# Optimization experiments

Measured on AMD Instinct MI355X. Metric: run time of the kernel, lower is better.

Reference implementation:

```python
import jax, jax.numpy as jnp
import numpy as np
import math

N = 768; C_S = 384; C_Z = 128; H = 12; C = 16; P_QK = 4; P_V = 8; C_Z4 = C_Z // 4
INF = 1e5; EPS = 1e-8; LN_EPS = 1e-5


def setup_inputs() -> dict:
    key = jax.random.key(0)
    ks = jax.random.split(key, 16)
    w = lambda k, shp, sc=0.02: jax.random.normal(k, shp, jnp.float32) * sc
    s = jax.random.normal(ks[0], (N, C_S), jnp.float32)
    z = jax.random.normal(ks[1], (N, N, C_Z), jnp.float32)
    m = jax.random.normal(ks[2], (N, 3, 3), jnp.float32)
    q, r_ = jnp.linalg.qr(m)
    rot = q * jnp.sign(jnp.diagonal(r_, axis1=-2, axis2=-1))[:, None, :]  # orthonormal frames
    trans = jax.random.normal(ks[3], (N, 3), jnp.float32) * 10.0
    return {
        "s": s, "z": z, "rot": rot, "trans": trans,
        "s_mask": jnp.ones((N,), jnp.float32),
        "g_s": jnp.ones((C_S,), jnp.float32), "b_s": jnp.zeros((C_S,), jnp.float32),
        "g_z": jnp.ones((C_Z,), jnp.float32), "b_z": jnp.zeros((C_Z,), jnp.float32),
        "Wq": w(ks[4], (C_S, H * C)), "Wk": w(ks[5], (C_S, H * C)), "Wv": w(ks[6], (C_S, H * C)),
        "Wqp": w(ks[7], (C_S, H * P_QK * 3)), "Wkp": w(ks[8], (C_S, H * P_QK * 3)),
        "Wvp": w(ks[9], (C_S, H * P_V * 3)),
        "Wb": w(ks[10], (C_Z, H)), "Wdz": w(ks[11], (C_Z, C_Z4)),
        "head_weights": jnp.zeros((H,), jnp.float32),
        "Wout": w(ks[12], (H * C, C_S)), "Woutb": w(ks[13], (H * C_Z4, C_S)),
        "Woutpts": w(ks[14], (H * P_V * 4, C_S)),
        "rigids_to_res_idx": jnp.arange(N, dtype=jnp.int32),
    }


def _ipa(s, z, rot, trans, s_mask, g_s, b_s, g_z, b_z, Wq, Wk, Wv, Wqp, Wkp, Wvp,
         Wb, Wdz, head_weights, Wout, Woutb, Woutpts, idx):
    def ln(x, g, b):
        mu = jnp.mean(x, -1, keepdims=True)
        var = jnp.mean((x - mu) ** 2, -1, keepdims=True)
        return (x - mu) * jax.lax.rsqrt(var + LN_EPS) * g + b

    s = ln(s, g_s, b_s)
    z = ln(z, g_z, b_z)
    n = s.shape[0]
    q = (s @ Wq).reshape(n, H, C)
    k = (s @ Wk).reshape(n, H, C)
    v = (s @ Wv).reshape(n, H, C)

    def to_global(pts):  # r.apply: R x + t, per residue
        return jnp.einsum('nij,npj->npi', rot, pts) + trans[:, None, :]

    q_pts = to_global((s @ Wqp).reshape(n, H * P_QK, 3))
    k_pts = to_global((s @ Wkp).reshape(n, H * P_QK, 3))
    v_pts = to_global((s @ Wvp).reshape(n, H * P_V, 3))

    b = z @ Wb                      # [N, N, H] pair bias
    pair_z = z @ Wdz                # [N, N, C_Z4]
    mask2 = s_mask[:, None] * s_mask[None, :]
    z_bias = b + (INF * (mask2 - 1.0))[..., None]
    z_bias = z_bias[idx][:, idx]    # broadcast z over rigids via rigid->res index
    pair_g = pair_z[idx][:, idx]

    qp = q_pts.reshape(n, H, P_QK, 3)
    kp = k_pts.reshape(n, H, P_QK, 3)
    d2 = jnp.sum((qp[:, None] - kp[None, :]) ** 2, -1)  # [N, N, H, P_QK]
    hw = jax.nn.softplus(head_weights) * math.sqrt(1.0 / (3 * (P_QK * 9.0 / 2)))
    pt_att = -0.5 * jnp.sum(d2, -1) * hw                # [N, N, H]

    a = (jnp.einsum('ihc,jhc->ijh', q, k) * math.sqrt(1.0 / (3 * C))
         + math.sqrt(1.0 / 3) * z_bias + pt_att)
    a = jax.nn.softmax(a, axis=1)                       # softmax over keys j

    o = jnp.einsum('ijh,jhc->ihc', a, v).reshape(n, H * C)
    vp = v_pts.reshape(n, H, P_V, 3)
    o_pt = jnp.einsum('ijh,jhpx->ihpx', a, vp).reshape(n, H * P_V, 3)
    o_pair = jnp.einsum('ijh,ijc->ihc', a, pair_g).reshape(n, H * C_Z4)

    # r.invert_apply: R^T (x - t)
    o_pt = jnp.einsum('nji,npj->npi', rot, o_pt - trans[:, None, :])
    o_pt_norm = jnp.sqrt(jnp.sum(o_pt ** 2, -1) + EPS)  # [N, H*P_V]
    pts_feat = jnp.concatenate([o_pt.reshape(n, -1), o_pt_norm], -1)
    return o @ Wout + o_pair @ Woutb + pts_feat @ Woutpts


def reference(s, z, rot, trans, s_mask, g_s, b_s, g_z, b_z, Wq, Wk, Wv, Wqp, Wkp, Wvp,
              Wb, Wdz, head_weights, Wout, Woutb, Woutpts, rigids_to_res_idx):
    return _ipa(s, z, rot, trans, s_mask, g_s, b_s, g_z, b_z, Wq, Wk, Wv, Wqp, Wkp,
                Wvp, Wb, Wdz, head_weights, Wout, Woutb, Woutpts, rigids_to_res_idx)
```

## Files before the change

### kernel.cpp

```cpp
#include <hip/hip_runtime.h>
#include <hip/hip_bf16.h>

#define NN 768
#define NSQ (768*768)
#define CS 384
#define CZ 128
#define HH 12
#define INF_ 1e5f
#define EPS_ 1e-8f
#define LN_EPS_ 1e-5f

typedef __attribute__((ext_vector_type(8))) short short8;
typedef __attribute__((ext_vector_type(4))) short short4_t;
typedef __attribute__((ext_vector_type(4))) float floatx4;

constexpr size_t OFF_SLN  = 0;
constexpr size_t OFF_PROJ = OFF_SLN + (size_t)768*384;
constexpr size_t OFF_QPG  = OFF_PROJ + (size_t)768*1152;
constexpr size_t OFF_KPG  = OFF_QPG + (size_t)768*144;
constexpr size_t OFF_VPG  = OFF_KPG + (size_t)768*144;
constexpr size_t OFF_WTBF = OFF_VPG + (size_t)768*288;
constexpr size_t OFF_HW   = OFF_WTBF + 4096;
constexpr size_t OFF_BIAS = OFF_HW + 16;
constexpr size_t OFF_ATT  = OFF_BIAS + (size_t)NSQ*6;
constexpr size_t OFF_PZ   = OFF_ATT + (size_t)12*NSQ;
constexpr size_t OFF_OCAT = OFF_PZ + (size_t)NSQ*16;

__device__ __forceinline__ unsigned short f2bf(float f){
    unsigned int u = __float_as_uint(f);
    u = (u + 0x7fffu + ((u >> 16) & 1u)) >> 16;
    return (unsigned short)u;
}
__device__ __forceinline__ float bf2f(unsigned short u){
    return __uint_as_float((unsigned int)u << 16);
}

__global__ __launch_bounds__(256) void k_setup(const float* __restrict__ Wb, const float* __restrict__ Wdz,
                                               const float* __restrict__ hwin, float* __restrict__ ws,
                                               float* __restrict__ out){
    int b = blockIdx.x, t = threadIdx.x;
    if (b < 2880){ ws[OFF_OCAT + (size_t)b*256 + t] = 0.f; return; }
    b -= 2880;
    if (b < 1152){ out[(size_t)b*256 + t] = 0.f; return; }
    b -= 1152;
    if (b < 24){
        unsigned short* wt = (unsigned short*)(ws + OFF_WTBF);
        int o = b*2 + (t>>7), k = t & 127;
        float v = 0.f;
        if (o < HH) v = Wb[k*HH + o];
        else if (o < 44) v = Wdz[k*32 + (o - HH)];
        wt[o*128 + k] = f2bf(v);
        return;
    }
    b -= 24;
    if (b == 0 && t < HH){
        ws[OFF_HW + t] = log1pf(expf(hwin[t])) * sqrtf(1.0f/54.0f);
    }
}

__global__ __launch_bounds__(128) void k_lns(const float* __restrict__ s, const float* __restrict__ g,
                                             const float* __restrict__ b, float* __restrict__ ws){
    int i = blockIdx.x, t = threadIdx.x;
    const float* row = s + (size_t)i*CS;
    float x0 = row[t], x1 = row[t+128], x2 = row[t+256];
    float sum = x0+x1+x2, sq = x0*x0+x1*x1+x2*x2;
    for (int off = 32; off; off >>= 1){ sum += __shfl_down(sum, off, 64); sq += __shfl_down(sq, off, 64); }
    __shared__ float ls[2][2];
    int w = t >> 6;
    if ((t & 63) == 0){ ls[w][0] = sum; ls[w][1] = sq; }
    __syncthreads();
    sum = ls[0][0] + ls[1][0]; sq = ls[0][1] + ls[1][1];
    float mu = sum * (1.0f/CS);
    float var = sq * (1.0f/CS) - mu*mu;
    float rstd = rsqrtf(var + LN_EPS_);
    float* outp = ws + OFF_SLN + (size_t)i*CS;
    outp[t]     = (x0-mu)*rstd*g[t]     + b[t];
    outp[t+128] = (x1-mu)*rstd*g[t+128] + b[t+128];
    outp[t+256] = (x2-mu)*rstd*g[t+256] + b[t+256];
}

__global__ __launch_bounds__(256) void k_proj(const float* __restrict__ Wq, const float* __restrict__ Wk,
                                              const float* __restrict__ Wv, const float* __restrict__ Wqp,
                                              const float* __restrict__ Wkp, const float* __restrict__ Wvp,
                                              float* __restrict__ ws){
    __shared__ float slds[16][CS];
    const float* sln = ws + OFF_SLN;
    int rt = blockIdx.x, ct = blockIdx.y, t = threadIdx.x;
    for (int ix = t; ix < 16*CS; ix += 256){
        int r = ix / CS, c = ix % CS;
        slds[r][c] = sln[(size_t)(rt*16 + r)*CS + c];
    }
    __syncthreads();
    int col = ct*128 + (t & 127);
    int rg = t >> 7;
    const float* wp; int stride;
    if      (col < 192){ wp = Wq  + col;       stride = 192; }
    else if (col < 384){ wp = Wk  + (col-192); stride = 192; }
    else if (col < 576){ wp = Wv  + (col-384); stride = 192; }
    else if (col < 720){ wp = Wqp + (col-576); stride = 144; }
    else if (col < 864){ wp = Wkp + (col-720); stride = 144; }
    else               { wp = Wvp + (col-864); stride = 288; }
    float acc[8] = {0,0,0,0,0,0,0,0};
    for (int k = 0; k < CS; k += 4){
        float w0 = wp[(size_t)k*stride];
        float w1 = wp[(size_t)(k+1)*stride];
        float w2 = wp[(size_t)(k+2)*stride];
        float w3 = wp[(size_t)(k+3)*stride];
        #pragma unroll
        for (int r = 0; r < 8; r++){
            floatx4 sv = *(const floatx4*)&slds[rg*8+r][k];
            acc[r] += sv[0]*w0 + sv[1]*w1 + sv[2]*w2 + sv[3]*w3;
        }
    }
    float* proj = ws + OFF_PROJ;
    for (int r = 0; r < 8; r++) proj[(size_t)(rt*16 + rg*8 + r)*1152 + col] = acc[r];
}

__global__ __launch_bounds__(192) void k_pts(const float* __restrict__ rot, const float* __restrict__ trans,
                                             float* __restrict__ ws){
    int i = blockIdx.x, p = threadIdx.x;
    const float* proj = ws + OFF_PROJ + (size_t)i*1152;
    const float* src; float* dst;
    if (p < 48)      { src = proj + 576 + p*3;       dst = ws + OFF_QPG + (size_t)i*144 + p*3; }
    else if (p < 96) { src = proj + 720 + (p-48)*3;  dst = ws + OFF_KPG + (size_t)i*144 + (p-48)*3; }
    else             { src = proj + 864 + (p-96)*3;  dst = ws + OFF_VPG + (size_t)i*288 + (p-96)*3; }
    float x = src[0], y = src[1], z = src[2];
    const float* R = rot + (size_t)i*9;
    const float* T = trans + (size_t)i*3;
    dst[0] = R[0]*x + R[1]*y + R[2]*z + T[0];
    dst[1] = R[3]*x + R[4]*y + R[5]*z + T[1];
    dst[2] = R[6]*x + R[7]*y + R[8]*z + T[2];
}

__global__ __launch_bounds__(256) void k_z(const float* __restrict__ z, const float* __restrict__ gz,
                                           const float* __restrict__ bz, float* __restrict__ ws){
    __shared__ unsigned short zlds[64][136];
    int t = threadIdx.x;
    int pb = blockIdx.x * 64;
    int lane32 = t & 31;
    int col = lane32 * 4;
    floatx4 g4 = *(const floatx4*)(gz + col);
    floatx4 b4 = *(const floatx4*)(bz + col);
    const float* zbase = z + (size_t)pb * 128;
    #pragma unroll
    for (int g = 0; g < 8; g++){
        int row = g*8 + (t >> 5);
        floatx4 v = *(const floatx4*)(zbase + (size_t)g*1024 + (size_t)t*4);
        float sum = v[0]+v[1]+v[2]+v[3];
        float sq  = v[0]*v[0]+v[1]*v[1]+v[2]*v[2]+v[3]*v[3];
        #pragma unroll
        for (int off = 1; off <= 16; off <<= 1){
            sum += __shfl_xor(sum, off, 64);
            sq  += __shfl_xor(sq , off, 64);
        }
        float mu = sum * (1.0f/128.0f);
        float rstd = rsqrtf(sq*(1.0f/128.0f) - mu*mu + LN_EPS_);
        short4_t sv;
        sv[0] = (short)f2bf((v[0]-mu)*rstd*g4[0] + b4[0]);
        sv[1] = (short)f2bf((v[1]-mu)*rstd*g4[1] + b4[1]);
        sv[2] = (short)f2bf((v[2]-mu)*rstd*g4[2] + b4[2]);
        sv[3] = (short)f2bf((v[3]-mu)*rstd*g4[3] + b4[3]);
        *(short4_t*)&zlds[row][col] = sv;
    }
    __syncthreads();
    const unsigned short* wt = (const unsigned short*)(ws + OFF_WTBF);
    int lane = t & 63, wv = t >> 6;
    int m = lane & 15, quad = lane >> 4;
    short8 bfrag[3][4];
    #pragma unroll
    for (int ot = 0; ot < 3; ot++)
        #pragma unroll
        for (int ks = 0; ks < 4; ks++){
            int o = ot*16 + m;
            bfrag[ot][ks] = *(const short8*)(wt + o*128 + ks*32 + quad*8);
        }
    floatx4 acc[3] = {{0.f,0.f,0.f,0.f},{0.f,0.f,0.f,0.f},{0.f,0.f,0.f,0.f}};
    int rbase = wv*16;
    #pragma unroll
    for (int ks = 0; ks < 4; ks++){
        short8 a = *(const short8*)&zlds[rbase + m][ks*32 + quad*8];
        acc[0] = __builtin_amdgcn_mfma_f32_16x16x32_bf16(a, bfrag[0][ks], acc[0], 0, 0, 0);
        acc[1] = __builtin_amdgcn_mfma_f32_16x16x32_bf16(a, bfrag[1][ks], acc[1], 0, 0, 0);
        acc[2] = __builtin_amdgcn_mfma_f32_16x16x32_bf16(a, bfrag[2][ks], acc[2], 0, 0, 0);
    }
    unsigned short* bias16 = (unsigned short*)(ws + OFF_BIAS);
    unsigned short* pz16   = (unsigned short*)(ws + OFF_PZ);
    #pragma unroll
    for (int ot = 0; ot < 3; ot++){
        int o = ot*16 + m;
        #pragma unroll
        for (int rg = 0; rg < 4; rg++){
            int pair = pb + rbase + quad*4 + rg;
            float val = acc[ot][rg];
            if (o < HH)      bias16[(size_t)o*NSQ + pair] = f2bf(val);
            else if (o < 44) pz16[(size_t)pair*32 + (o - HH)] = f2bf(val);
        }
    }
}

__global__ __launch_bounds__(256) void k_logits(const float* __restrict__ smask, const int* __restrict__ idx,
                                                float* __restrict__ ws){
    __shared__ float qlds[8][336];
    __shared__ float klds[32][338];
    int it = blockIdx.x, jt = blockIdx.y, t = threadIdx.x;
    const float* proj = ws + OFF_PROJ;
    const float* qpg  = ws + OFF_QPG;
    const float* kpg  = ws + OFF_KPG;
    const float* hw   = ws + OFF_HW;
    const unsigned short* bias16 = (const unsigned short*)(ws + OFF_BIAS);
    float* att = ws + OFF_ATT;
    for (int ix = t; ix < 8*336; ix += 256){
        int r = ix / 336, c = ix % 336;
        int i = it*8 + r;
        qlds[r][c] = (c < 192) ? proj[(size_t)i*1152 + c] : qpg[(size_t)i*144 + (c - 192)];
    }
    for (int ix = t; ix < 32*336; ix += 256){
        int r = ix / 336, c = ix % 336;
        int j = jt*32 + r;
        klds[r][c] = (c < 192) ? proj[(size_t)j*1152 + 192 + c] : kpg[(size_t)j*144 + (c - 192)];
    }
    __syncthreads();
    int jl = t & 31, grp = t >> 5;
    int i = it*8 + grp, j = jt*32 + jl;
    int ires = idx[i], jres = idx[j];
    float mterm = INF_ * (smask[ires]*smask[jres] - 1.0f);
    const float S1 = 0.14433756729740643f;
    const float S2 = 0.57735026918962576f;
    for (int h = 0; h < HH; h++){
        floatx4 q0 = *(const floatx4*)&qlds[grp][h*16];
        floatx4 q1 = *(const floatx4*)&qlds[grp][h*16+4];
        floatx4 q2 = *(const floatx4*)&qlds[grp][h*16+8];
        floatx4 q3 = *(const floatx4*)&qlds[grp][h*16+12];
        const float* kr = &klds[jl][h*16];
        float2 k0 = *(const float2*)(kr+0),  k1 = *(const float2*)(kr+2);
        float2 k2 = *(const float2*)(kr+4),  k3 = *(const float2*)(kr+6);
        float2 k4 = *(const float2*)(kr+8),  k5 = *(const float2*)(kr+10);
        float2 k6 = *(const float2*)(kr+12), k7 = *(const float2*)(kr+14);
        float qk = q0[0]*k0.x+q0[1]*k0.y+q0[2]*k1.x+q0[3]*k1.y
                 + q1[0]*k2.x+q1[1]*k2.y+q1[2]*k3.x+q1[3]*k3.y
                 + q2[0]*k4.x+q2[1]*k4.y+q2[2]*k5.x+q2[3]*k5.y
                 + q3[0]*k6.x+q3[1]*k6.y+q3[2]*k7.x+q3[3]*k7.y;
        floatx4 qp0 = *(const floatx4*)&qlds[grp][192+h*12];
        floatx4 qp1 = *(const floatx4*)&qlds[grp][192+h*12+4];
        floatx4 qp2 = *(const floatx4*)&qlds[grp][192+h*12+8];
        const float* kp = &klds[jl][192+h*12];
        float2 p0 = *(const float2*)(kp+0), p1 = *(const float2*)(kp+2);
        float2 p2 = *(const float2*)(kp+4), p3 = *(const float2*)(kp+6);
        float2 p4 = *(const float2*)(kp+8), p5 = *(const float2*)(kp+10);
        float d0 = qp0[0]-p0.x, d1 = qp0[1]-p0.y, d2a = qp0[2]-p1.x, d3 = qp0[3]-p1.y;
        float d4 = qp1[0]-p2.x, d5 = qp1[1]-p2.y, d6 = qp1[2]-p3.x, d7 = qp1[3]-p3.y;
        float d8 = qp2[0]-p4.x, d9 = qp2[1]-p4.y, dA = qp2[2]-p5.x, dB = qp2[3]-p5.y;
        float d2 = d0*d0+d1*d1+d2a*d2a+d3*d3 + d4*d4+d5*d5+d6*d6+d7*d7 + d8*d8+d9*d9+dA*dA+dB*dB;
        float bv = bf2f(bias16[(size_t)h*NSQ + (size_t)ires*NN + jres]);
        float lg = qk*S1 + S2*(bv + mterm) - 0.5f*hw[h]*d2;
        att[(size_t)h*NSQ + (size_t)i*NN + j] = lg;
    }
}

__global__ __launch_bounds__(192) void k_softmax(float* __restrict__ ws){
    int b = blockIdx.x, t = threadIdx.x;
    float* row = ws + OFF_ATT + (size_t)b*NN;
    floatx4 v = *(floatx4*)(row + t*4);
    float mx = fmaxf(fmaxf(v[0],v[1]), fmaxf(v[2],v[3]));
    for (int off = 32; off; off >>= 1) mx = fmaxf(mx, __shfl_xor(mx, off, 64));
    __shared__ float lsm[3];
    __shared__ float lss[3];
    int w = t >> 6;
    if ((t & 63) == 0) lsm[w] = mx;
    __syncthreads();
    mx = fmaxf(fmaxf(lsm[0], lsm[1]), lsm[2]);
    floatx4 e;
    e[0] = expf(v[0]-mx); e[1] = expf(v[1]-mx); e[2] = expf(v[2]-mx); e[3] = expf(v[3]-mx);
    float s = e[0]+e[1]+e[2]+e[3];
    for (int off = 32; off; off >>= 1) s += __shfl_xor(s, off, 64);
    if ((t & 63) == 0) lss[w] = s;
    __syncthreads();
    s = lss[0] + lss[1] + lss[2];
    float inv = 1.0f / s;
    e[0] *= inv; e[1] *= inv; e[2] *= inv; e[3] *= inv;
    *(floatx4*)(row + t*4) = e;
}

__global__ __launch_bounds__(256) void k_ov(float* __restrict__ ws){
    __shared__ float wlds[128][41];
    __shared__ float plds[32][128];
    int h = blockIdx.x, it = blockIdx.y, zs = blockIdx.z, t = threadIdx.x;
    const float* proj = ws + OFF_PROJ;
    const float* vpg  = ws + OFF_VPG;
    const float* att  = ws + OFF_ATT + (size_t)h*NSQ;
    int c = t & 63, isub = t >> 6;
    float acc[8] = {0,0,0,0,0,0,0,0};
    for (int jt = zs*2; jt < zs*2+2; jt++){
        __syncthreads();
        for (int ix = t; ix < 128*40; ix += 256){
            int jj = ix / 40, cc = ix % 40;
            int j = jt*128 + jj;
            wlds[jj][cc] = (cc < 16) ? proj[(size_t)j*1152 + 384 + h*16 + cc]
                                     : vpg[(size_t)j*288 + h*24 + (cc - 16)];
        }
        for (int ix = t; ix < 32*128; ix += 256){
            int rr = ix >> 7, jj = ix & 127;
            plds[rr][jj] = att[(size_t)(it*32 + rr)*NN + jt*128 + jj];
        }
        __syncthreads();
        if (c < 40){
            for (int jj = 0; jj < 128; jj += 4){
                float w0 = wlds[jj][c], w1 = wlds[jj+1][c], w2 = wlds[jj+2][c], w3 = wlds[jj+3][c];
                #pragma unroll
                for (int rr = 0; rr < 8; rr++){
                    floatx4 pv = *(floatx4*)&plds[isub*8+rr][jj];
                    acc[rr] += pv[0]*w0 + pv[1]*w1 + pv[2]*w2 + pv[3]*w3;
                }
            }
        }
    }
    if (c < 40){
        float* ocat = ws + OFF_OCAT;
        int col = (c < 16) ? (h*16 + c) : (576 + h*24 + (c - 16));
        for (int rr = 0; rr < 8; rr++){
            int i = it*32 + isub*8 + rr;
            atomicAdd(&ocat[(size_t)i*960 + col], acc[rr]);
        }
    }
}

__global__ __launch_bounds__(384) void k_opair(const int* __restrict__ idx, float* __restrict__ ws){
    __shared__ float plds[12][132];
    __shared__ float pzlds[128][33];
    int i = blockIdx.x, jt = blockIdx.y, t = threadIdx.x;
    int ires = idx[i];
    const unsigned int* pzg = (const unsigned int*)((const unsigned short*)(ws + OFF_PZ) + (size_t)ires*NN*32);
    const float* att = ws + OFF_ATT;
    for (int ix = t; ix < 12*128; ix += 384){
        int hh = ix >> 7, jj = ix & 127;
        plds[hh][jj] = att[(size_t)hh*NSQ + (size_t)i*NN + jt*128 + jj];
    }
    for (int ix = t; ix < 128*16; ix += 384){
        int jj = ix >> 4, cp = ix & 15;
        int jres = idx[jt*128 + jj];
        unsigned int u2 = pzg[(size_t)jres*16 + cp];
        pzlds[jj][cp*2]   = __uint_as_float(u2 << 16);
        pzlds[jj][cp*2+1] = __uint_as_float(u2 & 0xffff0000u);
    }
    __syncthreads();
    int h = t >> 5, c = t & 31;
    float acc = 0.f;
    #pragma unroll 4
    for (int j = 0; j < 128; j++)
        acc += plds[h][j] * pzlds[j][c];
    float* oc = ws + OFF_OCAT + (size_t)i*960 + 192;
    atomicAdd(&oc[h*32 + c], acc);
}

__global__ __launch_bounds__(96) void k_ptfin(const float* __restrict__ rot, const float* __restrict__ trans,
                                              float* __restrict__ ws){
    int i = blockIdx.x, p = threadIdx.x;
    float* base = ws + OFF_OCAT + (size_t)i*960;
    float* pt = base + 576 + p*3;
    float x = pt[0] - trans[i*3+0];
    float y = pt[1] - trans[i*3+1];
    float z = pt[2] - trans[i*3+2];
    const float* R = rot + (size_t)i*9;
    float lx = R[0]*x + R[3]*y + R[6]*z;
    float ly = R[1]*x + R[4]*y + R[7]*z;
    float lz = R[2]*x + R[5]*y + R[8]*z;
    pt[0] = lx; pt[1] = ly; pt[2] = lz;
    base[864 + p] = sqrtf(lx*lx + ly*ly + lz*lz + EPS_);
}

__global__ __launch_bounds__(256) void k_out(const float* __restrict__ Wout, const float* __restrict__ Woutb,
                                             const float* __restrict__ Woutp, float* __restrict__ ws,
                                             float* __restrict__ out){
    __shared__ float olds[32][244];
    int it = blockIdx.x, ct = blockIdx.y, kc = blockIdx.z, t = threadIdx.x;
    const float* ocat = ws + OFF_OCAT;
    for (int ix = t; ix < 32*240; ix += 256){
        int r = ix / 240, kk = ix % 240;
        olds[r][kk] = ocat[(size_t)(it*32 + r)*960 + kc*240 + kk];
    }
    __syncthreads();
    int cl = t & 63, ig = t >> 6;
    int c0 = ct*128 + cl, c1 = c0 + 64;
    float acc0[8], acc1[8];
    #pragma unroll
    for (int r=0;r<8;r++){ acc0[r]=0; acc1[r]=0; }
    for (int kk = 0; kk < 240; kk += 4){
        float w0[4], w1[4];
        #pragma unroll
        for (int u = 0; u < 4; u++){
            int k = kc*240 + kk + u;
            const float* wrow = (k < 192) ? (Wout  + (size_t)k*CS)
                              : (k < 576) ? (Woutb + (size_t)(k-192)*CS)
                                          : (Woutp + (size_t)(k-576)*CS);
            w0[u] = wrow[c0]; w1[u] = wrow[c1];
        }
        #pragma unroll
        for (int r = 0; r < 8; r++){
            floatx4 ov = *(const floatx4*)&olds[ig*8 + r][kk];
            acc0[r] += ov[0]*w0[0] + ov[1]*w0[1] + ov[2]*w0[2] + ov[3]*w0[3];
            acc1[r] += ov[0]*w1[0] + ov[1]*w1[1] + ov[2]*w1[2] + ov[3]*w1[3];
        }
    }
    for (int r = 0; r < 8; r++){
        int i = it*32 + ig*8 + r;
        atomicAdd(&out[(size_t)i*CS + c0], acc0[r]);
        atomicAdd(&out[(size_t)i*CS + c1], acc1[r]);
    }
}

extern "C" void kernel_launch(void* const* d_in, const int* in_sizes, int n_in,
                              void* d_out, int out_size, void* d_ws, size_t ws_size,
                              hipStream_t stream){
    const float* s     = (const float*)d_in[0];
    const float* z     = (const float*)d_in[1];
    const float* rot   = (const float*)d_in[2];
    const float* trans = (const float*)d_in[3];
    const float* smask = (const float*)d_in[4];
    const float* gs    = (const float*)d_in[5];
    const float* bs    = (const float*)d_in[6];
    const float* gz    = (const float*)d_in[7];
    const float* bz    = (const float*)d_in[8];
    const float* Wq    = (const float*)d_in[9];
    const float* Wk    = (const float*)d_in[10];
    const float* Wv    = (const float*)d_in[11];
    const float* Wqp   = (const float*)d_in[12];
    const float* Wkp   = (const float*)d_in[13];
    const float* Wvp   = (const float*)d_in[14];
    const float* Wb    = (const float*)d_in[15];
    const float* Wdz   = (const float*)d_in[16];
    const float* hwin  = (const float*)d_in[17];
    const float* Wout  = (const float*)d_in[18];
    const float* Woutb = (const float*)d_in[19];
    const float* Woutp = (const float*)d_in[20];
    const int*   idx   = (const int*)d_in[21];
    float* ws  = (float*)d_ws;
    float* out = (float*)d_out;

    k_setup  <<<4057, 256, 0, stream>>>(Wb, Wdz, hwin, ws, out);
    k_lns    <<<768, 128, 0, stream>>>(s, gs, bs, ws);
    k_proj   <<<dim3(48, 9), 256, 0, stream>>>(Wq, Wk, Wv, Wqp, Wkp, Wvp, ws);
    k_pts    <<<768, 192, 0, stream>>>(rot, trans, ws);
    k_z      <<<9216, 256, 0, stream>>>(z, gz, bz, ws);
    k_logits <<<dim3(96, 24), 256, 0, stream>>>(smask, idx, ws);
    k_softmax<<<9216, 192, 0, stream>>>(ws);
    k_ov     <<<dim3(12, 24, 3), 256, 0, stream>>>(ws);
    k_opair  <<<dim3(768, 6), 384, 0, stream>>>(idx, ws);
    k_ptfin  <<<768, 96, 0, stream>>>(rot, trans, ws);
    k_out    <<<dim3(24, 3, 4), 256, 0, stream>>>(Wout, Woutb, Woutp, ws, out);
}
```

Before: 810.4 us.

## Fuse s-LayerNorm into projection, stage z outputs in LDS, wave-per-row softmax

Three separate changes. The s LayerNorm kernel is removed and its work is folded into k_proj: each block normalizes its 16 rows in shared memory, recomputing the stats once per column tile. The k_z epilogue now stages bias and pair-z results in LDS and writes them back as packed 32-bit coalesced stores instead of scattered 16-bit stores. Softmax now handles one row per wavefront with four rows per block, which removes the shared-memory reductions and barriers.

```diff
diff --git a/kernel.cpp b/kernel.cpp
--- a/kernel.cpp
+++ b/kernel.cpp
@@ -58,37 +58,44 @@
     }
 }
 
-__global__ __launch_bounds__(128) void k_lns(const float* __restrict__ s, const float* __restrict__ g,
-                                             const float* __restrict__ b, float* __restrict__ ws){
-    int i = blockIdx.x, t = threadIdx.x;
-    const float* row = s + (size_t)i*CS;
-    float x0 = row[t], x1 = row[t+128], x2 = row[t+256];
-    float sum = x0+x1+x2, sq = x0*x0+x1*x1+x2*x2;
-    for (int off = 32; off; off >>= 1){ sum += __shfl_down(sum, off, 64); sq += __shfl_down(sq, off, 64); }
-    __shared__ float ls[2][2];
-    int w = t >> 6;
-    if ((t & 63) == 0){ ls[w][0] = sum; ls[w][1] = sq; }
-    __syncthreads();
-    sum = ls[0][0] + ls[1][0]; sq = ls[0][1] + ls[1][1];
-    float mu = sum * (1.0f/CS);
-    float var = sq * (1.0f/CS) - mu*mu;
-    float rstd = rsqrtf(var + LN_EPS_);
-    float* outp = ws + OFF_SLN + (size_t)i*CS;
-    outp[t]     = (x0-mu)*rstd*g[t]     + b[t];
-    outp[t+128] = (x1-mu)*rstd*g[t+128] + b[t+128];
-    outp[t+256] = (x2-mu)*rstd*g[t+256] + b[t+256];
-}
-
-__global__ __launch_bounds__(256) void k_proj(const float* __restrict__ Wq, const float* __restrict__ Wk,
+__global__ __launch_bounds__(256) void k_proj(const float* __restrict__ s, const float* __restrict__ gs,
+                                              const float* __restrict__ bs,
+                                              const float* __restrict__ Wq, const float* __restrict__ Wk,
                                               const float* __restrict__ Wv, const float* __restrict__ Wqp,
                                               const float* __restrict__ Wkp, const float* __restrict__ Wvp,
                                               float* __restrict__ ws){
     __shared__ float slds[16][CS];
-    const float* sln = ws + OFF_SLN;
+    __shared__ float stats[16][2];
     int rt = blockIdx.x, ct = blockIdx.y, t = threadIdx.x;
     for (int ix = t; ix < 16*CS; ix += 256){
         int r = ix / CS, c = ix % CS;
-        slds[r][c] = sln[(size_t)(rt*16 + r)*CS + c];
+        slds[r][c] = s[(size_t)(rt*16 + r)*CS + c];
+    }
+    __syncthreads();
+    int w = t >> 6, lane = t & 63;
+    for (int r = w; r < 16; r += 4){
+        float sum = 0.f, sq = 0.f;
+        #pragma unroll
+        for (int c0 = 0; c0 < CS; c0 += 64){
+            float x = slds[r][c0 + lane];
+            sum += x; sq += x*x;
+        }
+        #pragma unroll
+        for (int off = 32; off; off >>= 1){
+            sum += __shfl_xor(sum, off, 64);
+            sq  += __shfl_xor(sq , off, 64);
+        }
+        if (lane == 0){
+            float mu = sum * (1.0f/CS);
+            float var = sq * (1.0f/CS) - mu*mu;
+            stats[r][0] = mu;
+            stats[r][1] = rsqrtf(var + LN_EPS_);
+        }
+    }
+    __syncthreads();
+    for (int ix = t; ix < 16*CS; ix += 256){
+        int r = ix / CS, c = ix % CS;
+        slds[r][c] = (slds[r][c] - stats[r][0]) * stats[r][1] * gs[c] + bs[c];
     }
     __syncthreads();
     int col = ct*128 + (t & 127);
@@ -183,18 +190,32 @@
         acc[1] = __builtin_amdgcn_mfma_f32_16x16x32_bf16(a, bfrag[1][ks], acc[1], 0, 0, 0);
         acc[2] = __builtin_amdgcn_mfma_f32_16x16x32_bf16(a, bfrag[2][ks], acc[2], 0, 0, 0);
     }
-    unsigned short* bias16 = (unsigned short*)(ws + OFF_BIAS);
-    unsigned short* pz16   = (unsigned short*)(ws + OFF_PZ);
+    __syncthreads();
+    unsigned short* stb = &zlds[0][0];
+    unsigned short* stp = &zlds[0][0] + 64*12;
     #pragma unroll
     for (int ot = 0; ot < 3; ot++){
         int o = ot*16 + m;
         #pragma unroll
         for (int rg = 0; rg < 4; rg++){
-            int pair = pb + rbase + quad*4 + rg;
+            int rp = rbase + quad*4 + rg;
             float val = acc[ot][rg];
-            if (o < HH)      bias16[(size_t)o*NSQ + pair] = f2bf(val);
-            else if (o < 44) pz16[(size_t)pair*32 + (o - HH)] = f2bf(val);
-        }
+            if (o < HH)      stb[rp*12 + o] = f2bf(val);
+            else if (o < 44) stp[rp*32 + (o - HH)] = f2bf(val);
+        }
+    }
+    __syncthreads();
+    unsigned short* bias16 = (unsigned short*)(ws + OFF_BIAS);
+    unsigned int*   pz32   = (unsigned int*)((unsigned short*)(ws + OFF_PZ));
+    for (int ix = t; ix < 12*32; ix += 256){
+        int o = ix >> 5, u = ix & 31;
+        unsigned int val = (unsigned int)stb[(u*2)*12 + o] | ((unsigned int)stb[(u*2+1)*12 + o] << 16);
+        *(unsigned int*)(bias16 + (size_t)o*NSQ + pb + u*2) = val;
+    }
+    for (int ix = t; ix < 64*16; ix += 256){
+        int rp = ix >> 4, u = ix & 15;
+        unsigned int val = (unsigned int)stp[rp*32 + u*2] | ((unsigned int)stp[rp*32 + u*2+1] << 16);
+        pz32[(size_t)(pb + rp)*16 + u] = val;
     }
 }
 
@@ -257,28 +278,31 @@
     }
 }
 
-__global__ __launch_bounds__(192) void k_softmax(float* __restrict__ ws){
-    int b = blockIdx.x, t = threadIdx.x;
-    float* row = ws + OFF_ATT + (size_t)b*NN;
-    floatx4 v = *(floatx4*)(row + t*4);
-    float mx = fmaxf(fmaxf(v[0],v[1]), fmaxf(v[2],v[3]));
+__global__ __launch_bounds__(256) void k_softmax(float* __restrict__ ws){
+    int t = threadIdx.x;
+    int w = t >> 6, lane = t & 63;
+    size_t rowi = (size_t)blockIdx.x*4 + w;
+    float* row = ws + OFF_ATT + rowi*NN;
+    floatx4 v0 = *(floatx4*)(row + lane*4);
+    floatx4 v1 = *(floatx4*)(row + 256 + lane*4);
+    floatx4 v2 = *(floatx4*)(row + 512 + lane*4);
+    float mx = fmaxf(fmaxf(fmaxf(v0[0],v0[1]), fmaxf(v0[2],v0[3])),
+               fmaxf(fmaxf(fmaxf(v1[0],v1[1]), fmaxf(v1[2],v1[3])),
+                     fmaxf(fmaxf(v2[0],v2[1]), fmaxf(v2[2],v2[3]))));
+    #pragma unroll
     for (int off = 32; off; off >>= 1) mx = fmaxf(mx, __shfl_xor(mx, off, 64));
-    __shared__ float lsm[3];
-    __shared__ float lss[3];
-    int w = t >> 6;
-    if ((t & 63) == 0) lsm[w] = mx;
-    __syncthreads();
-    mx = fmaxf(fmaxf(lsm[0], lsm[1]), lsm[2]);
-    floatx4 e;
-    e[0] = expf(v[0]-mx); e[1] = expf(v[1]-mx); e[2] = expf(v[2]-mx); e[3] = expf(v[3]-mx);
-    float s = e[0]+e[1]+e[2]+e[3];
+    floatx4 e0, e1, e2;
+    #pragma unroll
+    for (int u = 0; u < 4; u++){ e0[u] = expf(v0[u]-mx); e1[u] = expf(v1[u]-mx); e2[u] = expf(v2[u]-mx); }
+    float s = e0[0]+e0[1]+e0[2]+e0[3] + e1[0]+e1[1]+e1[2]+e1[3] + e2[0]+e2[1]+e2[2]+e2[3];
+    #pragma unroll
     for (int off = 32; off; off >>= 1) s += __shfl_xor(s, off, 64);
-    if ((t & 63) == 0) lss[w] = s;
-    __syncthreads();
-    s = lss[0] + lss[1] + lss[2];
     float inv = 1.0f / s;
-    e[0] *= inv; e[1] *= inv; e[2] *= inv; e[3] *= inv;
-    *(floatx4*)(row + t*4) = e;
+    #pragma unroll
+    for (int u = 0; u < 4; u++){ e0[u] *= inv; e1[u] *= inv; e2[u] *= inv; }
+    *(floatx4*)(row + lane*4) = e0;
+    *(floatx4*)(row + 256 + lane*4) = e1;
+    *(floatx4*)(row + 512 + lane*4) = e2;
 }
 
 __global__ __launch_bounds__(256) void k_ov(float* __restrict__ ws){
@@ -437,12 +461,11 @@
     float* out = (float*)d_out;
 
     k_setup  <<<4057, 256, 0, stream>>>(Wb, Wdz, hwin, ws, out);
-    k_lns    <<<768, 128, 0, stream>>>(s, gs, bs, ws);
-    k_proj   <<<dim3(48, 9), 256, 0, stream>>>(Wq, Wk, Wv, Wqp, Wkp, Wvp, ws);
+    k_proj   <<<dim3(48, 9), 256, 0, stream>>>(s, gs, bs, Wq, Wk, Wv, Wqp, Wkp, Wvp, ws);
     k_pts    <<<768, 192, 0, stream>>>(rot, trans, ws);
     k_z      <<<9216, 256, 0, stream>>>(z, gz, bz, ws);
     k_logits <<<dim3(96, 24), 256, 0, stream>>>(smask, idx, ws);
-    k_softmax<<<9216, 192, 0, stream>>>(ws);
+    k_softmax<<<2304, 256, 0, stream>>>(ws);
     k_ov     <<<dim3(12, 24, 3), 256, 0, stream>>>(ws);
     k_opair  <<<dim3(768, 6), 384, 0, stream>>>(idx, ws);
     k_ptfin  <<<768, 96, 0, stream>>>(rot, trans, ws);
```

After: 793.4 us. 1.02x faster.
